# Optimization experiments

Measured on AMD Instinct MI355X. Metric: run time of the kernel, lower is better.

## Reference

```python
import jax, jax.numpy as jnp
import numpy as np

N_NODES = 50000
N_EDGES = 800000
D = 128  # in_dim == hidden_dim


def setup_inputs() -> dict:
    key = jax.random.key(0)
    k1, k2, k3, k4 = jax.random.split(key, 4)
    x = jax.random.normal(k1, (N_NODES, D), dtype=jnp.float32)
    edge_index = jax.random.randint(k2, (2, N_EDGES), 0, N_NODES, dtype=jnp.int64)
    # Glorot-ish scale for square weights
    scale = 1.0 / np.sqrt(D)
    W1 = jax.random.normal(k3, (D, D), dtype=jnp.float32) * scale
    W2 = jax.random.normal(k4, (D, D), dtype=jnp.float32) * scale
    b1 = jnp.zeros((D,), dtype=jnp.float32)
    b2 = jnp.zeros((D,), dtype=jnp.float32)
    return {"x": x, "edge_index": edge_index, "W1": W1, "b1": b1, "W2": W2, "b2": b2}


def _gcn_layer(x, W, b, src, dst, norm, n):
    # PyG GCNConv: h = x @ W, then symmetric-normalized scatter-add, then + bias
    h = x @ W                                   # [N, D] dense GEMM
    msg = h[src] * norm[:, None]                # [E', D] gather + scale
    out = jax.ops.segment_sum(msg, dst, num_segments=n)  # scatter-add
    return out + b


def reference(x, edge_index, W1, b1, W2, b2):
    n = x.shape[0]
    # add self-loops (GCNConv default add_self_loops=True)
    loops = jnp.arange(n, dtype=edge_index.dtype)
    src = jnp.concatenate([edge_index[0], loops])
    dst = jnp.concatenate([edge_index[1], loops])
    # symmetric normalization: deg^{-1/2}[src] * deg^{-1/2}[dst]
    deg = jax.ops.segment_sum(jnp.ones_like(src, dtype=x.dtype), dst, num_segments=n)
    dinv = jax.lax.rsqrt(jnp.maximum(deg, 1.0))  # deg >= 1 due to self-loops
    norm = dinv[src] * dinv[dst]
    # layer 1: conv -> relu (dropout is identity in eval mode)
    h = jax.nn.relu(_gcn_layer(x, W1, b1, src, dst, norm, n))
    # layer 2 (cut='c2'): conv -> relu
    h = jax.nn.relu(_gcn_layer(h, W2, b2, src, dst, norm, n))
    return h
```

## Files before the change

### kernel.cpp

```cpp
#include <hip/hip_runtime.h>

#define NN 50000
#define NE 800000
#define DD 128
#define NSTRIP 3125
#define NB 196
#define CHUNK 4096
#define MAXB 6144

#define OF_BCUR  0
#define OF_DINV  256
#define OF_OFFS2 50432
#define OF_TMP   150528
#define OF_CSRU  1723392
#define OF_G1    2509824
#define OF_G2    5709824
#define OF_W1H   8909824
#define OF_W1L   8918016
#define OF_W2H   8926208
#define OF_W2L   8934400

typedef __attribute__((ext_vector_type(8))) short bf8_t;
typedef __attribute__((ext_vector_type(8))) unsigned short us8;
typedef __attribute__((ext_vector_type(4))) float f32x4;

static __device__ __forceinline__ unsigned short f2bf(float f) {
    unsigned int u = __float_as_uint(f);
    unsigned int r = (u + 0x7fffu + ((u >> 16) & 1u)) >> 16;
    return (unsigned short)r;
}
static __device__ __forceinline__ float bf2f(unsigned short h) {
    return __uint_as_float(((unsigned int)h) << 16);
}

__global__ void k_wconv(const float* __restrict__ W1, const float* __restrict__ W2,
                        ushort* __restrict__ w1h, ushort* __restrict__ w1l,
                        ushort* __restrict__ w2h, ushort* __restrict__ w2l,
                        int* __restrict__ bcur) {
    if (blockIdx.x == 0) bcur[threadIdx.x] = 0;
    int gg = blockIdx.x * 256 + threadIdx.x;
    const float* W = (gg < 2048) ? W1 : W2;
    ushort* wh = (gg < 2048) ? w1h : w2h;
    ushort* wl = (gg < 2048) ? w1l : w2l;
    int g = gg & 2047;
    int ntile = g >> 8;
    int kk = (g >> 6) & 3;
    int lane = g & 63;
    int k0 = kk * 32 + ((lane >> 4) * 8);
    int col = ntile * 16 + (lane & 15);
#pragma unroll
    for (int j = 0; j < 8; ++j) {
        float w = W[(k0 + j) * DD + col];
        unsigned short h = f2bf(w);
        wh[(size_t)g * 8 + j] = h;
        wl[(size_t)g * 8 + j] = f2bf(w - bf2f(h));
    }
}

__global__ void k_shuf(const int* __restrict__ src, const int* __restrict__ dst,
                       int* __restrict__ bcur, unsigned int* __restrict__ tmp) {
    __shared__ int lcnt[256];
    __shared__ int lbase[256];
    __shared__ int lcur[256];
    int tid = threadIdx.x;
    lcnt[tid] = 0;
    __syncthreads();
    int e0 = blockIdx.x * CHUNK;
    int e1 = e0 + CHUNK; if (e1 > NE) e1 = NE;
    for (int e = e0 + tid; e < e1; e += 256)
        atomicAdd(&lcnt[dst[e] >> 8], 1);
    __syncthreads();
    if (lcnt[tid]) lbase[tid] = atomicAdd(&bcur[tid], lcnt[tid]);
    lcur[tid] = 0;
    __syncthreads();
    for (int e = e0 + tid; e < e1; e += 256) {
        int d = dst[e], s = src[e];
        int b = d >> 8;
        int r = atomicAdd(&lcur[b], 1);
        tmp[(size_t)b * MAXB + lbase[b] + r] =
            ((unsigned int)s << 8) | (unsigned int)(d & 255);
    }
}

__global__ __launch_bounds__(256) void k_sort(const int* __restrict__ bcur,
                                              const unsigned int* __restrict__ tmp,
                                              ushort* __restrict__ csru,
                                              int2* __restrict__ offs2,
                                              float* __restrict__ dinv) {
    __shared__ unsigned int ent[MAXB];
    __shared__ int cnt[256];
    __shared__ int boff[256];
    __shared__ int cur[256];
    int b = blockIdx.x, tid = threadIdx.x;
    int base = b * MAXB;
    int nb = bcur[b];
    cnt[tid] = 0;
    __syncthreads();
    for (int i = tid; i < nb; i += 256) {
        unsigned int v = tmp[base + i];
        ent[i] = v;
        atomicAdd(&cnt[v & 255], 1);
    }
    __syncthreads();
    int v = cnt[tid];
    boff[tid] = v;
    __syncthreads();
    for (int o = 1; o < 256; o <<= 1) {
        int t = (tid >= o) ? boff[tid - o] : 0;
        __syncthreads();
        boff[tid] += t;
        __syncthreads();
    }
    int excl = boff[tid] - v;
    int node = b * 256 + tid;
    if (node < NN) {
        offs2[node] = make_int2(base + excl, base + excl + v);
        dinv[node] = rsqrtf((float)(v + 1));
    }
    cur[tid] = excl;
    __syncthreads();
    for (int i = tid; i < nb; i += 256) {
        unsigned int e = ent[i];
        int bin = e & 255;
        int r = atomicAdd(&cur[bin], 1);
        csru[base + r] = (ushort)(e >> 8);
    }
}

__global__ __launch_bounds__(256) void k_mgemm(const float* __restrict__ X,
                                               const ushort* __restrict__ wh,
                                               const ushort* __restrict__ wl,
                                               const float* __restrict__ dinv,
                                               ushort* __restrict__ G) {
    int wave = threadIdx.x >> 6;
    int lane = threadIdx.x & 63;
    int strip = blockIdx.x * 4 + wave;
    if (strip >= NSTRIP) return;
    int rb = strip << 4;
    int m = lane & 15;
    int quad = lane >> 4;
    const float* ar = X + (size_t)(rb + m) * DD;
    f32x4 acc[8];
#pragma unroll
    for (int t = 0; t < 8; ++t) acc[t] = (f32x4){0.f, 0.f, 0.f, 0.f};
#pragma unroll
    for (int kk = 0; kk < 4; ++kk) {
        float4 xa = *(const float4*)(ar + kk * 32 + quad * 8);
        float4 xb = *(const float4*)(ar + kk * 32 + quad * 8 + 4);
        float xs[8] = {xa.x, xa.y, xa.z, xa.w, xb.x, xb.y, xb.z, xb.w};
        bf8_t ah, al;
#pragma unroll
        for (int j = 0; j < 8; ++j) {
            unsigned short hh = f2bf(xs[j]);
            ah[j] = (short)hh;
            al[j] = (short)f2bf(xs[j] - bf2f(hh));
        }
#pragma unroll
        for (int t = 0; t < 8; ++t) {
            size_t bo = ((size_t)(t * 4 + kk) * 64 + lane) * 8;
            bf8_t bh = *(const bf8_t*)(wh + bo);
            bf8_t bl = *(const bf8_t*)(wl + bo);
            acc[t] = __builtin_amdgcn_mfma_f32_16x16x32_bf16(ah, bh, acc[t], 0, 0, 0);
            acc[t] = __builtin_amdgcn_mfma_f32_16x16x32_bf16(ah, bl, acc[t], 0, 0, 0);
            acc[t] = __builtin_amdgcn_mfma_f32_16x16x32_bf16(al, bh, acc[t], 0, 0, 0);
        }
    }
    float dv[4];
#pragma unroll
    for (int r = 0; r < 4; ++r) dv[r] = dinv[rb + quad * 4 + r];
#pragma unroll
    for (int t = 0; t < 8; ++t) {
#pragma unroll
        for (int r = 0; r < 4; ++r)
            G[(size_t)(rb + quad * 4 + r) * DD + t * 16 + m] = f2bf(dv[r] * acc[t][r]);
    }
}

__global__ __launch_bounds__(256) void k_aggmm(const ushort* __restrict__ g1,
                                               const float* __restrict__ dinv,
                                               const int2* __restrict__ offs2,
                                               const ushort* __restrict__ csru,
                                               const float* __restrict__ b1,
                                               const ushort* __restrict__ w2h,
                                               const ushort* __restrict__ w2l,
                                               ushort* __restrict__ g2) {
    __shared__ float xs[16][132];
    int wave = threadIdx.x >> 6;
    int lane = threadIdx.x & 63;
    int rb = blockIdx.x * 16;
    int q = lane >> 4;
    int l = lane & 15;
    const float* bp = b1 + 8 * l;
    for (int nn = 0; nn < 4; ++nn) {
        int node = rb + wave * 4 + nn;
        float a0[8] = {0.f, 0.f, 0.f, 0.f, 0.f, 0.f, 0.f, 0.f};
        float a1[8] = {0.f, 0.f, 0.f, 0.f, 0.f, 0.f, 0.f, 0.f};
        float a2[8] = {0.f, 0.f, 0.f, 0.f, 0.f, 0.f, 0.f, 0.f};
        float a3[8] = {0.f, 0.f, 0.f, 0.f, 0.f, 0.f, 0.f, 0.f};
        int2 oe = offs2[node];
        int e  = oe.x + q;
        int e1 = oe.y;
        for (; e + 12 < e1; e += 16) {
            int s0 = csru[e];
            int s1 = csru[e + 4];
            int s2 = csru[e + 8];
            int s3 = csru[e + 12];
            us8 v0 = *(const us8*)(g1 + (size_t)s0 * DD + 8 * l);
            us8 v1 = *(const us8*)(g1 + (size_t)s1 * DD + 8 * l);
            us8 v2 = *(const us8*)(g1 + (size_t)s2 * DD + 8 * l);
            us8 v3 = *(const us8*)(g1 + (size_t)s3 * DD + 8 * l);
#pragma unroll
            for (int j = 0; j < 8; ++j) {
                a0[j] += bf2f(v0[j]);
                a1[j] += bf2f(v1[j]);
                a2[j] += bf2f(v2[j]);
                a3[j] += bf2f(v3[j]);
            }
        }
        for (; e < e1; e += 4) {
            int s0 = csru[e];
            us8 v0 = *(const us8*)(g1 + (size_t)s0 * DD + 8 * l);
#pragma unroll
            for (int j = 0; j < 8; ++j) a0[j] += bf2f(v0[j]);
        }
        if (q == 0) {
            us8 v = *(const us8*)(g1 + (size_t)node * DD + 8 * l);
#pragma unroll
            for (int j = 0; j < 8; ++j) a0[j] += bf2f(v[j]);
        }
#pragma unroll
        for (int j = 0; j < 8; ++j) {
            a0[j] += a1[j] + a2[j] + a3[j];
            a0[j] += __shfl_xor(a0[j], 16, 64);
            a0[j] += __shfl_xor(a0[j], 32, 64);
        }
        if (q == 0) {
            float di = dinv[node];
            float* xr = &xs[wave * 4 + nn][8 * l];
#pragma unroll
            for (int j = 0; j < 8; ++j)
                xr[j] = fmaxf(di * a0[j] + bp[j], 0.f);
        }
    }
    __syncthreads();
    int m = lane & 15;
    int quad = lane >> 4;
    f32x4 acc[2];
    acc[0] = (f32x4){0.f, 0.f, 0.f, 0.f};
    acc[1] = (f32x4){0.f, 0.f, 0.f, 0.f};
#pragma unroll
    for (int kk = 0; kk < 4; ++kk) {
        const float* xr = &xs[m][kk * 32 + quad * 8];
        float4 xa = *(const float4*)xr;
        float4 xb = *(const float4*)(xr + 4);
        float xv[8] = {xa.x, xa.y, xa.z, xa.w, xb.x, xb.y, xb.z, xb.w};
        bf8_t ah, al;
#pragma unroll
        for (int j = 0; j < 8; ++j) {
            unsigned short hh = f2bf(xv[j]);
            ah[j] = (short)hh;
            al[j] = (short)f2bf(xv[j] - bf2f(hh));
        }
#pragma unroll
        for (int tt = 0; tt < 2; ++tt) {
            int t = wave * 2 + tt;
            size_t bo = ((size_t)(t * 4 + kk) * 64 + lane) * 8;
            bf8_t bh = *(const bf8_t*)(w2h + bo);
            bf8_t bl = *(const bf8_t*)(w2l + bo);
            acc[tt] = __builtin_amdgcn_mfma_f32_16x16x32_bf16(ah, bh, acc[tt], 0, 0, 0);
            acc[tt] = __builtin_amdgcn_mfma_f32_16x16x32_bf16(ah, bl, acc[tt], 0, 0, 0);
            acc[tt] = __builtin_amdgcn_mfma_f32_16x16x32_bf16(al, bh, acc[tt], 0, 0, 0);
        }
    }
    float dv[4];
#pragma unroll
    for (int r = 0; r < 4; ++r) dv[r] = dinv[rb + quad * 4 + r];
#pragma unroll
    for (int tt = 0; tt < 2; ++tt) {
        int t = wave * 2 + tt;
#pragma unroll
        for (int r = 0; r < 4; ++r)
            g2[(size_t)(rb + quad * 4 + r) * DD + t * 16 + m] = f2bf(dv[r] * acc[tt][r]);
    }
}

__global__ void k_agg(const ushort* __restrict__ g, const float* __restrict__ dinv,
                      const int2* __restrict__ offs2, const ushort* __restrict__ csru,
                      const float* __restrict__ bias, float* __restrict__ outf) {
    int wave = threadIdx.x >> 6;
    int lane = threadIdx.x & 63;
    int node = blockIdx.x * 4 + wave;
    int q = lane >> 4;
    int l = lane & 15;
    float a0[8] = {0.f, 0.f, 0.f, 0.f, 0.f, 0.f, 0.f, 0.f};
    float a1[8] = {0.f, 0.f, 0.f, 0.f, 0.f, 0.f, 0.f, 0.f};
    float a2[8] = {0.f, 0.f, 0.f, 0.f, 0.f, 0.f, 0.f, 0.f};
    float a3[8] = {0.f, 0.f, 0.f, 0.f, 0.f, 0.f, 0.f, 0.f};
    int2 oe = offs2[node];
    int e  = oe.x + q;
    int e1 = oe.y;
    for (; e + 12 < e1; e += 16) {
        int s0 = csru[e];
        int s1 = csru[e + 4];
        int s2 = csru[e + 8];
        int s3 = csru[e + 12];
        us8 v0 = *(const us8*)(g + (size_t)s0 * DD + 8 * l);
        us8 v1 = *(const us8*)(g + (size_t)s1 * DD + 8 * l);
        us8 v2 = *(const us8*)(g + (size_t)s2 * DD + 8 * l);
        us8 v3 = *(const us8*)(g + (size_t)s3 * DD + 8 * l);
#pragma unroll
        for (int j = 0; j < 8; ++j) {
            a0[j] += bf2f(v0[j]);
            a1[j] += bf2f(v1[j]);
            a2[j] += bf2f(v2[j]);
            a3[j] += bf2f(v3[j]);
        }
    }
    for (; e < e1; e += 4) {
        int s0 = csru[e];
        us8 v0 = *(const us8*)(g + (size_t)s0 * DD + 8 * l);
#pragma unroll
        for (int j = 0; j < 8; ++j) a0[j] += bf2f(v0[j]);
    }
    if (q == 0) {
        us8 v = *(const us8*)(g + (size_t)node * DD + 8 * l);
#pragma unroll
        for (int j = 0; j < 8; ++j) a0[j] += bf2f(v[j]);
    }
#pragma unroll
    for (int j = 0; j < 8; ++j) {
        a0[j] += a1[j] + a2[j] + a3[j];
        a0[j] += __shfl_xor(a0[j], 16, 64);
        a0[j] += __shfl_xor(a0[j], 32, 64);
    }
    if (q == 0) {
        float di = dinv[node];
        float* op = outf + (size_t)node * DD + 8 * l;
        const float* bp = bias + 8 * l;
        float4 o0, o1;
        o0.x = fmaxf(di * a0[0] + bp[0], 0.f);
        o0.y = fmaxf(di * a0[1] + bp[1], 0.f);
        o0.z = fmaxf(di * a0[2] + bp[2], 0.f);
        o0.w = fmaxf(di * a0[3] + bp[3], 0.f);
        o1.x = fmaxf(di * a0[4] + bp[4], 0.f);
        o1.y = fmaxf(di * a0[5] + bp[5], 0.f);
        o1.z = fmaxf(di * a0[6] + bp[6], 0.f);
        o1.w = fmaxf(di * a0[7] + bp[7], 0.f);
        *(float4*)op = o0;
        *(float4*)(op + 4) = o1;
    }
}

extern "C" void kernel_launch(void* const* d_in, const int* in_sizes, int n_in,
                              void* d_out, int out_size, void* d_ws, size_t ws_size,
                              hipStream_t stream) {
    const float* x  = (const float*)d_in[0];
    const int*   ei = (const int*)d_in[1];
    const float* W1 = (const float*)d_in[2];
    const float* b1 = (const float*)d_in[3];
    const float* W2 = (const float*)d_in[4];
    const float* b2 = (const float*)d_in[5];
    float* out = (float*)d_out;

    const int* src = ei;
    const int* dst = ei + NE;

    int*          wsi  = (int*)d_ws;
    float*        wsf  = (float*)d_ws;
    ushort*       wsu  = (ushort*)d_ws;
    unsigned int* wsuw = (unsigned int*)d_ws;
    int*    bcur  = wsi + OF_BCUR;
    float*  dinv  = wsf + OF_DINV;
    int2*   offs2 = (int2*)(wsi + OF_OFFS2);
    unsigned int* tmp = wsuw + OF_TMP;
    ushort* csru  = wsu + (size_t)OF_CSRU * 2;
    ushort* g1    = wsu + (size_t)OF_G1 * 2;
    ushort* g2    = wsu + (size_t)OF_G2 * 2;
    ushort* w1h   = wsu + (size_t)OF_W1H * 2;
    ushort* w1l   = wsu + (size_t)OF_W1L * 2;
    ushort* w2h   = wsu + (size_t)OF_W2H * 2;
    ushort* w2l   = wsu + (size_t)OF_W2L * 2;

    const int chunks = (NE + CHUNK - 1) / CHUNK;

    hipLaunchKernelGGL(k_wconv, dim3(16), dim3(256), 0, stream,
                       W1, W2, w1h, w1l, w2h, w2l, bcur);
    hipLaunchKernelGGL(k_shuf,  dim3(chunks), dim3(256), 0, stream, src, dst, bcur, tmp);
    hipLaunchKernelGGL(k_sort,  dim3(NB), dim3(256), 0, stream, bcur, tmp, csru, offs2, dinv);

    const int gblocks = (NSTRIP + 3) / 4;

    hipLaunchKernelGGL(k_mgemm, dim3(gblocks), dim3(256), 0, stream, x, w1h, w1l, dinv, g1);
    hipLaunchKernelGGL(k_aggmm, dim3(NSTRIP), dim3(256), 0, stream,
                       g1, dinv, offs2, csru, b1, w2h, w2l, g2);
    hipLaunchKernelGGL(k_agg,   dim3(NN / 4), dim3(256), 0, stream,
                       g2, dinv, offs2, csru, b2, out);
}
```

Measured before the change: 214.1 us.

## Merge edge bucketing with layer-1 GEMM, drop global atomics, rescale by source dinv

The edge bucketing pass and the first dense GEMM now run in one launch. Blocks 0-195 bucket the edges and the rest compute X@W1, so the graph preprocessing overlaps the matmul. Bucketing no longer uses global atomic counters: each chunk writes local counts and offsets, and k_sort rebuilds its bucket with a prefix scan plus a binary search over the chunks. Because the GEMM no longer knows dinv, the source-side normalization moves into the gather loops as a per-edge dinv[s] multiply, and k_aggmm uses 512 threads with one output tile per wave. In exchange, every gathered edge now does an extra scalar load and multiply, and the sort pass reads scattered chunk segments.

Result: faster. 208.0 us (-2.8%).

```diff
diff --git a/kernel.cpp b/kernel.cpp
--- a/kernel.cpp
+++ b/kernel.cpp
@@ -8,17 +8,18 @@
 #define CHUNK 4096
 #define MAXB 6144
 
-#define OF_BCUR  0
-#define OF_DINV  256
-#define OF_OFFS2 50432
-#define OF_TMP   150528
-#define OF_CSRU  1723392
-#define OF_G1    2509824
-#define OF_G2    5709824
-#define OF_W1H   8909824
-#define OF_W1L   8918016
-#define OF_W2H   8926208
-#define OF_W2L   8934400
+#define OF_LCNT  0
+#define OF_LOFS  50176
+#define OF_DINV  100352
+#define OF_OFFS2 150528
+#define OF_TMP2  250624
+#define OF_CSRU  1053440
+#define OF_H1    1655552
+#define OF_H2    4855552
+#define OF_W1H   8055552
+#define OF_W1L   8063744
+#define OF_W2H   8071936
+#define OF_W2L   8080128
 
 typedef __attribute__((ext_vector_type(8))) short bf8_t;
 typedef __attribute__((ext_vector_type(8))) unsigned short us8;
@@ -35,9 +36,7 @@
 
 __global__ void k_wconv(const float* __restrict__ W1, const float* __restrict__ W2,
                         ushort* __restrict__ w1h, ushort* __restrict__ w1l,
-                        ushort* __restrict__ w2h, ushort* __restrict__ w2l,
-                        int* __restrict__ bcur) {
-    if (blockIdx.x == 0) bcur[threadIdx.x] = 0;
+                        ushort* __restrict__ w2h, ushort* __restrict__ w2l) {
     int gg = blockIdx.x * 256 + threadIdx.x;
     const float* W = (gg < 2048) ? W1 : W2;
     ushort* wh = (gg < 2048) ? w1h : w2h;
@@ -57,61 +56,141 @@
     }
 }
 
-__global__ void k_shuf(const int* __restrict__ src, const int* __restrict__ dst,
-                       int* __restrict__ bcur, unsigned int* __restrict__ tmp) {
+__global__ __launch_bounds__(256) void k_prep(
+        const int* __restrict__ src, const int* __restrict__ dst,
+        int* __restrict__ lcnt_g, int* __restrict__ lofs_g,
+        unsigned int* __restrict__ tmp2,
+        const float* __restrict__ X,
+        const ushort* __restrict__ wh, const ushort* __restrict__ wl,
+        ushort* __restrict__ H1) {
     __shared__ int lcnt[256];
-    __shared__ int lbase[256];
+    __shared__ int lsc[256];
     __shared__ int lcur[256];
     int tid = threadIdx.x;
-    lcnt[tid] = 0;
-    __syncthreads();
-    int e0 = blockIdx.x * CHUNK;
-    int e1 = e0 + CHUNK; if (e1 > NE) e1 = NE;
-    for (int e = e0 + tid; e < e1; e += 256)
-        atomicAdd(&lcnt[dst[e] >> 8], 1);
-    __syncthreads();
-    if (lcnt[tid]) lbase[tid] = atomicAdd(&bcur[tid], lcnt[tid]);
-    lcur[tid] = 0;
-    __syncthreads();
-    for (int e = e0 + tid; e < e1; e += 256) {
-        int d = dst[e], s = src[e];
-        int b = d >> 8;
-        int r = atomicAdd(&lcur[b], 1);
-        tmp[(size_t)b * MAXB + lbase[b] + r] =
-            ((unsigned int)s << 8) | (unsigned int)(d & 255);
-    }
-}
-
-__global__ __launch_bounds__(256) void k_sort(const int* __restrict__ bcur,
-                                              const unsigned int* __restrict__ tmp,
+    if (blockIdx.x < 196) {
+        int blk = blockIdx.x;
+        lcnt[tid] = 0;
+        __syncthreads();
+        int e0 = blk * CHUNK;
+        int e1 = e0 + CHUNK; if (e1 > NE) e1 = NE;
+        for (int e = e0 + tid; e < e1; e += 256)
+            atomicAdd(&lcnt[dst[e] >> 8], 1);
+        __syncthreads();
+        int v = lcnt[tid];
+        lsc[tid] = v;
+        __syncthreads();
+        for (int o = 1; o < 256; o <<= 1) {
+            int t = (tid >= o) ? lsc[tid - o] : 0;
+            __syncthreads();
+            lsc[tid] += t;
+            __syncthreads();
+        }
+        int excl = lsc[tid] - v;
+        lcnt_g[tid * 196 + blk] = v;
+        lofs_g[tid * 196 + blk] = excl;
+        lcur[tid] = excl;
+        __syncthreads();
+        for (int e = e0 + tid; e < e1; e += 256) {
+            int d = dst[e], s = src[e];
+            int b = d >> 8;
+            int r = atomicAdd(&lcur[b], 1);
+            tmp2[blk * CHUNK + r] = ((unsigned int)s << 8) | (unsigned int)(d & 255);
+        }
+        return;
+    }
+    int wave = tid >> 6;
+    int lane = tid & 63;
+    int strip = (blockIdx.x - 196) * 4 + wave;
+    if (strip >= NSTRIP) return;
+    int rb = strip << 4;
+    int m = lane & 15;
+    int quad = lane >> 4;
+    const float* ar = X + (size_t)(rb + m) * DD;
+    f32x4 acc[8];
+#pragma unroll
+    for (int t = 0; t < 8; ++t) acc[t] = (f32x4){0.f, 0.f, 0.f, 0.f};
+#pragma unroll
+    for (int kk = 0; kk < 4; ++kk) {
+        float4 xa = *(const float4*)(ar + kk * 32 + quad * 8);
+        float4 xb = *(const float4*)(ar + kk * 32 + quad * 8 + 4);
+        float xs[8] = {xa.x, xa.y, xa.z, xa.w, xb.x, xb.y, xb.z, xb.w};
+        bf8_t ah, al;
+#pragma unroll
+        for (int j = 0; j < 8; ++j) {
+            unsigned short hh = f2bf(xs[j]);
+            ah[j] = (short)hh;
+            al[j] = (short)f2bf(xs[j] - bf2f(hh));
+        }
+#pragma unroll
+        for (int t = 0; t < 8; ++t) {
+            size_t bo = ((size_t)(t * 4 + kk) * 64 + lane) * 8;
+            bf8_t bh = *(const bf8_t*)(wh + bo);
+            bf8_t bl = *(const bf8_t*)(wl + bo);
+            acc[t] = __builtin_amdgcn_mfma_f32_16x16x32_bf16(ah, bh, acc[t], 0, 0, 0);
+            acc[t] = __builtin_amdgcn_mfma_f32_16x16x32_bf16(ah, bl, acc[t], 0, 0, 0);
+            acc[t] = __builtin_amdgcn_mfma_f32_16x16x32_bf16(al, bh, acc[t], 0, 0, 0);
+        }
+    }
+#pragma unroll
+    for (int t = 0; t < 8; ++t) {
+#pragma unroll
+        for (int r = 0; r < 4; ++r)
+            H1[(size_t)(rb + quad * 4 + r) * DD + t * 16 + m] = f2bf(acc[t][r]);
+    }
+}
+
+__global__ __launch_bounds__(256) void k_sort(const int* __restrict__ lcnt_g,
+                                              const int* __restrict__ lofs_g,
+                                              const unsigned int* __restrict__ tmp2,
                                               ushort* __restrict__ csru,
                                               int2* __restrict__ offs2,
                                               float* __restrict__ dinv) {
     __shared__ unsigned int ent[MAXB];
+    __shared__ int c[256];
+    __shared__ int p[256];
+    __shared__ int o[256];
     __shared__ int cnt[256];
     __shared__ int boff[256];
     __shared__ int cur[256];
     int b = blockIdx.x, tid = threadIdx.x;
-    int base = b * MAXB;
-    int nb = bcur[b];
+    int cv = (tid < 196) ? lcnt_g[b * 196 + tid] : 0;
+    o[tid] = (tid < 196) ? lofs_g[b * 196 + tid] : 0;
+    c[tid] = cv;
+    p[tid] = cv;
     cnt[tid] = 0;
     __syncthreads();
+    for (int s = 1; s < 256; s <<= 1) {
+        int t = (tid >= s) ? p[tid - s] : 0;
+        __syncthreads();
+        p[tid] += t;
+        __syncthreads();
+    }
+    int nb = p[255];
     for (int i = tid; i < nb; i += 256) {
-        unsigned int v = tmp[base + i];
-        ent[i] = v;
-        atomicAdd(&cnt[v & 255], 1);
+        int lo = 0, hi = 255;
+#pragma unroll
+        for (int it = 0; it < 8; ++it) {
+            int mid = (lo + hi) >> 1;
+            if (p[mid] > i) hi = mid; else lo = mid + 1;
+        }
+        int blk = lo;
+        int j = i - (p[blk] - c[blk]);
+        unsigned int e = tmp2[blk * CHUNK + o[blk] + j];
+        ent[i] = e;
+        atomicAdd(&cnt[e & 255], 1);
     }
     __syncthreads();
     int v = cnt[tid];
     boff[tid] = v;
     __syncthreads();
-    for (int o = 1; o < 256; o <<= 1) {
-        int t = (tid >= o) ? boff[tid - o] : 0;
+    for (int s = 1; s < 256; s <<= 1) {
+        int t = (tid >= s) ? boff[tid - s] : 0;
         __syncthreads();
         boff[tid] += t;
         __syncthreads();
     }
     int excl = boff[tid] - v;
+    int base = b * MAXB;
     int node = b * 256 + tid;
     if (node < NN) {
         offs2[node] = make_int2(base + excl, base + excl + v);
@@ -127,72 +206,23 @@
     }
 }
 
-__global__ __launch_bounds__(256) void k_mgemm(const float* __restrict__ X,
-                                               const ushort* __restrict__ wh,
-                                               const ushort* __restrict__ wl,
-                                               const float* __restrict__ dinv,
-                                               ushort* __restrict__ G) {
-    int wave = threadIdx.x >> 6;
-    int lane = threadIdx.x & 63;
-    int strip = blockIdx.x * 4 + wave;
-    if (strip >= NSTRIP) return;
-    int rb = strip << 4;
-    int m = lane & 15;
-    int quad = lane >> 4;
-    const float* ar = X + (size_t)(rb + m) * DD;
-    f32x4 acc[8];
-#pragma unroll
-    for (int t = 0; t < 8; ++t) acc[t] = (f32x4){0.f, 0.f, 0.f, 0.f};
-#pragma unroll
-    for (int kk = 0; kk < 4; ++kk) {
-        float4 xa = *(const float4*)(ar + kk * 32 + quad * 8);
-        float4 xb = *(const float4*)(ar + kk * 32 + quad * 8 + 4);
-        float xs[8] = {xa.x, xa.y, xa.z, xa.w, xb.x, xb.y, xb.z, xb.w};
-        bf8_t ah, al;
-#pragma unroll
-        for (int j = 0; j < 8; ++j) {
-            unsigned short hh = f2bf(xs[j]);
-            ah[j] = (short)hh;
-            al[j] = (short)f2bf(xs[j] - bf2f(hh));
-        }
-#pragma unroll
-        for (int t = 0; t < 8; ++t) {
-            size_t bo = ((size_t)(t * 4 + kk) * 64 + lane) * 8;
-            bf8_t bh = *(const bf8_t*)(wh + bo);
-            bf8_t bl = *(const bf8_t*)(wl + bo);
-            acc[t] = __builtin_amdgcn_mfma_f32_16x16x32_bf16(ah, bh, acc[t], 0, 0, 0);
-            acc[t] = __builtin_amdgcn_mfma_f32_16x16x32_bf16(ah, bl, acc[t], 0, 0, 0);
-            acc[t] = __builtin_amdgcn_mfma_f32_16x16x32_bf16(al, bh, acc[t], 0, 0, 0);
-        }
-    }
-    float dv[4];
-#pragma unroll
-    for (int r = 0; r < 4; ++r) dv[r] = dinv[rb + quad * 4 + r];
-#pragma unroll
-    for (int t = 0; t < 8; ++t) {
-#pragma unroll
-        for (int r = 0; r < 4; ++r)
-            G[(size_t)(rb + quad * 4 + r) * DD + t * 16 + m] = f2bf(dv[r] * acc[t][r]);
-    }
-}
-
-__global__ __launch_bounds__(256) void k_aggmm(const ushort* __restrict__ g1,
+__global__ __launch_bounds__(512) void k_aggmm(const ushort* __restrict__ h1,
                                                const float* __restrict__ dinv,
                                                const int2* __restrict__ offs2,
                                                const ushort* __restrict__ csru,
                                                const float* __restrict__ b1,
                                                const ushort* __restrict__ w2h,
                                                const ushort* __restrict__ w2l,
-                                               ushort* __restrict__ g2) {
-    __shared__ float xs[16][132];
+                                               ushort* __restrict__ h2) {
+    __shared__ float xs[16][136];
     int wave = threadIdx.x >> 6;
     int lane = threadIdx.x & 63;
     int rb = blockIdx.x * 16;
     int q = lane >> 4;
     int l = lane & 15;
     const float* bp = b1 + 8 * l;
-    for (int nn = 0; nn < 4; ++nn) {
-        int node = rb + wave * 4 + nn;
+    for (int nn = 0; nn < 2; ++nn) {
+        int node = rb + wave * 2 + nn;
         float a0[8] = {0.f, 0.f, 0.f, 0.f, 0.f, 0.f, 0.f, 0.f};
         float a1[8] = {0.f, 0.f, 0.f, 0.f, 0.f, 0.f, 0.f, 0.f};
         float a2[8] = {0.f, 0.f, 0.f, 0.f, 0.f, 0.f, 0.f, 0.f};
@@ -205,28 +235,31 @@
             int s1 = csru[e + 4];
             int s2 = csru[e + 8];
             int s3 = csru[e + 12];
-            us8 v0 = *(const us8*)(g1 + (size_t)s0 * DD + 8 * l);
-            us8 v1 = *(const us8*)(g1 + (size_t)s1 * DD + 8 * l);
-            us8 v2 = *(const us8*)(g1 + (size_t)s2 * DD + 8 * l);
-            us8 v3 = *(const us8*)(g1 + (size_t)s3 * DD + 8 * l);
+            float w0 = dinv[s0], w1 = dinv[s1], w2 = dinv[s2], w3 = dinv[s3];
+            us8 v0 = *(const us8*)(h1 + (size_t)s0 * DD + 8 * l);
+            us8 v1 = *(const us8*)(h1 + (size_t)s1 * DD + 8 * l);
+            us8 v2 = *(const us8*)(h1 + (size_t)s2 * DD + 8 * l);
+            us8 v3 = *(const us8*)(h1 + (size_t)s3 * DD + 8 * l);
 #pragma unroll
             for (int j = 0; j < 8; ++j) {
-                a0[j] += bf2f(v0[j]);
-                a1[j] += bf2f(v1[j]);
-                a2[j] += bf2f(v2[j]);
-                a3[j] += bf2f(v3[j]);
+                a0[j] += w0 * bf2f(v0[j]);
+                a1[j] += w1 * bf2f(v1[j]);
+                a2[j] += w2 * bf2f(v2[j]);
+                a3[j] += w3 * bf2f(v3[j]);
             }
         }
         for (; e < e1; e += 4) {
             int s0 = csru[e];
-            us8 v0 = *(const us8*)(g1 + (size_t)s0 * DD + 8 * l);
-#pragma unroll
-            for (int j = 0; j < 8; ++j) a0[j] += bf2f(v0[j]);
-        }
+            float w0 = dinv[s0];
+            us8 v0 = *(const us8*)(h1 + (size_t)s0 * DD + 8 * l);
+#pragma unroll
+            for (int j = 0; j < 8; ++j) a0[j] += w0 * bf2f(v0[j]);
+        }
+        float dnode = dinv[node];
         if (q == 0) {
-            us8 v = *(const us8*)(g1 + (size_t)node * DD + 8 * l);
-#pragma unroll
-            for (int j = 0; j < 8; ++j) a0[j] += bf2f(v[j]);
+            us8 v = *(const us8*)(h1 + (size_t)node * DD + 8 * l);
+#pragma unroll
+            for (int j = 0; j < 8; ++j) a0[j] += dnode * bf2f(v[j]);
         }
 #pragma unroll
         for (int j = 0; j < 8; ++j) {
@@ -235,19 +268,17 @@
             a0[j] += __shfl_xor(a0[j], 32, 64);
         }
         if (q == 0) {
-            float di = dinv[node];
-            float* xr = &xs[wave * 4 + nn][8 * l];
+            float* xr = &xs[wave * 2 + nn][8 * l];
 #pragma unroll
             for (int j = 0; j < 8; ++j)
-                xr[j] = fmaxf(di * a0[j] + bp[j], 0.f);
+                xr[j] = fmaxf(dnode * a0[j] + bp[j], 0.f);
         }
     }
     __syncthreads();
     int m = lane & 15;
     int quad = lane >> 4;
-    f32x4 acc[2];
-    acc[0] = (f32x4){0.f, 0.f, 0.f, 0.f};
-    acc[1] = (f32x4){0.f, 0.f, 0.f, 0.f};
+    int t = wave;
+    f32x4 acc = (f32x4){0.f, 0.f, 0.f, 0.f};
 #pragma unroll
     for (int kk = 0; kk < 4; ++kk) {
         const float* xr = &xs[m][kk * 32 + quad * 8];
@@ -261,30 +292,19 @@
             ah[j] = (short)hh;
             al[j] = (short)f2bf(xv[j] - bf2f(hh));
         }
-#pragma unroll
-        for (int tt = 0; tt < 2; ++tt) {
-            int t = wave * 2 + tt;
-            size_t bo = ((size_t)(t * 4 + kk) * 64 + lane) * 8;
-            bf8_t bh = *(const bf8_t*)(w2h + bo);
-            bf8_t bl = *(const bf8_t*)(w2l + bo);
-            acc[tt] = __builtin_amdgcn_mfma_f32_16x16x32_bf16(ah, bh, acc[tt], 0, 0, 0);
-            acc[tt] = __builtin_amdgcn_mfma_f32_16x16x32_bf16(ah, bl, acc[tt], 0, 0, 0);
-            acc[tt] = __builtin_amdgcn_mfma_f32_16x16x32_bf16(al, bh, acc[tt], 0, 0, 0);
-        }
-    }
-    float dv[4];
-#pragma unroll
-    for (int r = 0; r < 4; ++r) dv[r] = dinv[rb + quad * 4 + r];
-#pragma unroll
-    for (int tt = 0; tt < 2; ++tt) {
-        int t = wave * 2 + tt;
-#pragma unroll
-        for (int r = 0; r < 4; ++r)
-            g2[(size_t)(rb + quad * 4 + r) * DD + t * 16 + m] = f2bf(dv[r] * acc[tt][r]);
-    }
-}
-
-__global__ void k_agg(const ushort* __restrict__ g, const float* __restrict__ dinv,
+        size_t bo = ((size_t)(t * 4 + kk) * 64 + lane) * 8;
+        bf8_t bh = *(const bf8_t*)(w2h + bo);
+        bf8_t bl = *(const bf8_t*)(w2l + bo);
+        acc = __builtin_amdgcn_mfma_f32_16x16x32_bf16(ah, bh, acc, 0, 0, 0);
+        acc = __builtin_amdgcn_mfma_f32_16x16x32_bf16(ah, bl, acc, 0, 0, 0);
+        acc = __builtin_amdgcn_mfma_f32_16x16x32_bf16(al, bh, acc, 0, 0, 0);
+    }
+#pragma unroll
+    for (int r = 0; r < 4; ++r)
+        h2[(size_t)(rb + quad * 4 + r) * DD + t * 16 + m] = f2bf(acc[r]);
+}
+
+__global__ void k_agg(const ushort* __restrict__ h, const float* __restrict__ dinv,
                       const int2* __restrict__ offs2, const ushort* __restrict__ csru,
                       const float* __restrict__ bias, float* __restrict__ outf) {
     int wave = threadIdx.x >> 6;
@@ -304,28 +324,31 @@
         int s1 = csru[e + 4];
         int s2 = csru[e + 8];
         int s3 = csru[e + 12];
-        us8 v0 = *(const us8*)(g + (size_t)s0 * DD + 8 * l);
-        us8 v1 = *(const us8*)(g + (size_t)s1 * DD + 8 * l);
-        us8 v2 = *(const us8*)(g + (size_t)s2 * DD + 8 * l);
-        us8 v3 = *(const us8*)(g + (size_t)s3 * DD + 8 * l);
+        float w0 = dinv[s0], w1 = dinv[s1], w2 = dinv[s2], w3 = dinv[s3];
+        us8 v0 = *(const us8*)(h + (size_t)s0 * DD + 8 * l);
+        us8 v1 = *(const us8*)(h + (size_t)s1 * DD + 8 * l);
+        us8 v2 = *(const us8*)(h + (size_t)s2 * DD + 8 * l);
+        us8 v3 = *(const us8*)(h + (size_t)s3 * DD + 8 * l);
 #pragma unroll
         for (int j = 0; j < 8; ++j) {
-            a0[j] += bf2f(v0[j]);
-            a1[j] += bf2f(v1[j]);
-            a2[j] += bf2f(v2[j]);
-            a3[j] += bf2f(v3[j]);
+            a0[j] += w0 * bf2f(v0[j]);
+            a1[j] += w1 * bf2f(v1[j]);
+            a2[j] += w2 * bf2f(v2[j]);
+            a3[j] += w3 * bf2f(v3[j]);
         }
     }
     for (; e < e1; e += 4) {
         int s0 = csru[e];
-        us8 v0 = *(const us8*)(g + (size_t)s0 * DD + 8 * l);
-#pragma unroll
-        for (int j = 0; j < 8; ++j) a0[j] += bf2f(v0[j]);
-    }
+        float w0 = dinv[s0];
+        us8 v0 = *(const us8*)(h + (size_t)s0 * DD + 8 * l);
+#pragma unroll
+        for (int j = 0; j < 8; ++j) a0[j] += w0 * bf2f(v0[j]);
+    }
+    float dnode = dinv[node];
     if (q == 0) {
-        us8 v = *(const us8*)(g + (size_t)node * DD + 8 * l);
-#pragma unroll
-        for (int j = 0; j < 8; ++j) a0[j] += bf2f(v[j]);
+        us8 v = *(const us8*)(h + (size_t)node * DD + 8 * l);
+#pragma unroll
+        for (int j = 0; j < 8; ++j) a0[j] += dnode * bf2f(v[j]);
     }
 #pragma unroll
     for (int j = 0; j < 8; ++j) {
@@ -334,18 +357,17 @@
         a0[j] += __shfl_xor(a0[j], 32, 64);
     }
     if (q == 0) {
-        float di = dinv[node];
         float* op = outf + (size_t)node * DD + 8 * l;
         const float* bp = bias + 8 * l;
         float4 o0, o1;
-        o0.x = fmaxf(di * a0[0] + bp[0], 0.f);
-        o0.y = fmaxf(di * a0[1] + bp[1], 0.f);
-        o0.z = fmaxf(di * a0[2] + bp[2], 0.f);
-        o0.w = fmaxf(di * a0[3] + bp[3], 0.f);
-        o1.x = fmaxf(di * a0[4] + bp[4], 0.f);
-        o1.y = fmaxf(di * a0[5] + bp[5], 0.f);
-        o1.z = fmaxf(di * a0[6] + bp[6], 0.f);
-        o1.w = fmaxf(di * a0[7] + bp[7], 0.f);
+        o0.x = fmaxf(dnode * a0[0] + bp[0], 0.f);
+        o0.y = fmaxf(dnode * a0[1] + bp[1], 0.f);
+        o0.z = fmaxf(dnode * a0[2] + bp[2], 0.f);
+        o0.w = fmaxf(dnode * a0[3] + bp[3], 0.f);
+        o1.x = fmaxf(dnode * a0[4] + bp[4], 0.f);
+        o1.y = fmaxf(dnode * a0[5] + bp[5], 0.f);
+        o1.z = fmaxf(dnode * a0[6] + bp[6], 0.f);
+        o1.w = fmaxf(dnode * a0[7] + bp[7], 0.f);
         *(float4*)op = o0;
         *(float4*)(op + 4) = o1;
     }
@@ -369,30 +391,27 @@
     float*        wsf  = (float*)d_ws;
     ushort*       wsu  = (ushort*)d_ws;
     unsigned int* wsuw = (unsigned int*)d_ws;
-    int*    bcur  = wsi + OF_BCUR;
-    float*  dinv  = wsf + OF_DINV;
-    int2*   offs2 = (int2*)(wsi + OF_OFFS2);
-    unsigned int* tmp = wsuw + OF_TMP;
-    ushort* csru  = wsu + (size_t)OF_CSRU * 2;
-    ushort* g1    = wsu + (size_t)OF_G1 * 2;
-    ushort* g2    = wsu + (size_t)OF_G2 * 2;
-    ushort* w1h   = wsu + (size_t)OF_W1H * 2;
-    ushort* w1l   = wsu + (size_t)OF_W1L * 2;
-    ushort* w2h   = wsu + (size_t)OF_W2H * 2;
-    ushort* w2l   = wsu + (size_t)OF_W2L * 2;
-
-    const int chunks = (NE + CHUNK - 1) / CHUNK;
+    int*    lcnt_g = wsi + OF_LCNT;
+    int*    lofs_g = wsi + OF_LOFS;
+    float*  dinv   = wsf + OF_DINV;
+    int2*   offs2  = (int2*)(wsi + OF_OFFS2);
+    unsigned int* tmp2 = wsuw + OF_TMP2;
+    ushort* csru   = wsu + (size_t)OF_CSRU * 2;
+    ushort* h1     = wsu + (size_t)OF_H1 * 2;
+    ushort* h2     = wsu + (size_t)OF_H2 * 2;
+    ushort* w1h    = wsu + (size_t)OF_W1H * 2;
+    ushort* w1l    = wsu + (size_t)OF_W1L * 2;
+    ushort* w2h    = wsu + (size_t)OF_W2H * 2;
+    ushort* w2l    = wsu + (size_t)OF_W2L * 2;
 
     hipLaunchKernelGGL(k_wconv, dim3(16), dim3(256), 0, stream,
-                       W1, W2, w1h, w1l, w2h, w2l, bcur);
-    hipLaunchKernelGGL(k_shuf,  dim3(chunks), dim3(256), 0, stream, src, dst, bcur, tmp);
-    hipLaunchKernelGGL(k_sort,  dim3(NB), dim3(256), 0, stream, bcur, tmp, csru, offs2, dinv);
-
-    const int gblocks = (NSTRIP + 3) / 4;
-
-    hipLaunchKernelGGL(k_mgemm, dim3(gblocks), dim3(256), 0, stream, x, w1h, w1l, dinv, g1);
-    hipLaunchKernelGGL(k_aggmm, dim3(NSTRIP), dim3(256), 0, stream,
-                       g1, dinv, offs2, csru, b1, w2h, w2l, g2);
-    hipLaunchKernelGGL(k_agg,   dim3(NN / 4), dim3(256), 0, stream,
-                       g2, dinv, offs2, csru, b2, out);
-}
+                       W1, W2, w1h, w1l, w2h, w2l);
+    hipLaunchKernelGGL(k_prep, dim3(196 + (NSTRIP + 3) / 4), dim3(256), 0, stream,
+                       src, dst, lcnt_g, lofs_g, tmp2, x, w1h, w1l, h1);
+    hipLaunchKernelGGL(k_sort, dim3(NB), dim3(256), 0, stream,
+                       lcnt_g, lofs_g, tmp2, csru, offs2, dinv);
+    hipLaunchKernelGGL(k_aggmm, dim3(NSTRIP), dim3(512), 0, stream,
+                       h1, dinv, offs2, csru, b1, w2h, w2l, h2);
+    hipLaunchKernelGGL(k_agg, dim3(NN / 4), dim3(256), 0, stream,
+                       h2, dinv, offs2, csru, b2, out);
+}
```
